# Performance work log

Measured on AMD Instinct MI355X. Metric: run time of the kernel, lower is better.

## Reference

```python
import jax, jax.numpy as jnp
import numpy as np

B, INDIM, OUTDIM = 1024, 2048, 4096


def setup_inputs() -> dict:
    key = jax.random.key(0)
    kx, kw, kb = jax.random.split(key, 3)
    x = jax.random.normal(kx, (B, INDIM), dtype=jnp.float32)
    # nn.Linear(indim, outdim): weight [outdim, indim], bias [outdim]
    bound = 1.0 / np.sqrt(INDIM)
    W = jax.random.uniform(kw, (OUTDIM, INDIM), minval=-bound, maxval=bound, dtype=jnp.float32)
    b = jax.random.uniform(kb, (OUTDIM,), minval=-bound, maxval=bound, dtype=jnp.float32)
    return {"x": x, "W": W, "b": b}


def reference(x, W, b):
    # Faithful to torch: prototypes = weight.transpose(0,1).reshape(outdim, indim)
    # (a reflatten of W^T, not the original weight rows, since outdim != indim).
    protos = W.T.reshape(W.shape[0], W.shape[1])  # [outdim, indim]
    # -||x_i - p_j||^2 - b_j via GEMM identity (same math as broadcast subtract + norm^2)
    x_sq = jnp.sum(x * x, axis=1, keepdims=True)          # [B, 1]
    p_sq = jnp.sum(protos * protos, axis=1)[None, :]      # [1, outdim]
    xp = jnp.einsum('bd,od->bo', x, protos)               # [B, outdim]
    return -(x_sq - 2.0 * xp + p_sq) - b[None, :]
```

## Files before the change

kernel.cpp:

```cpp
#include <hip/hip_runtime.h>

#define IN_DIM  2048
#define OUT_DIM 4096

typedef float     f32x4 __attribute__((ext_vector_type(4)));
typedef long long llx2  __attribute__((ext_vector_type(2)));

__device__ __forceinline__ unsigned int pk4(float a, float b, float c, float d) {
    int v = __builtin_amdgcn_cvt_pk_fp8_f32(a, b, 0, false);
    v     = __builtin_amdgcn_cvt_pk_fp8_f32(c, d, v, true);
    return (unsigned int)v;
}

__device__ __forceinline__ void async16(const void* g, void* l) {
    __builtin_amdgcn_global_load_lds(
        (const __attribute__((address_space(1))) unsigned int*)g,
        (__attribute__((address_space(3))) unsigned int*)l,
        16, 0, 0);
}

__device__ __forceinline__ int gmem_of(int c) { return 2 * (c & 3) + (c >> 2); }

extern "C" __global__ __launch_bounds__(256) void prep(
        const float* __restrict__ W, const float* __restrict__ x,
        unsigned char* __restrict__ protos, unsigned char* __restrict__ xb,
        float* __restrict__ psq_part, float* __restrict__ x_sq) {
    __shared__ float tile[64][65];
    const int t = threadIdx.x;

    if (blockIdx.z == 2) {
        const int b = blockIdx.x + 32 * blockIdx.y;
        const float* xp = x + (size_t)b * IN_DIM + t * 8;
        const float4 v0 = ((const float4*)xp)[0];
        const float4 v1 = ((const float4*)xp)[1];
        uint2 pk;
        pk.x = pk4(v0.x, v0.y, v0.z, v0.w);
        pk.y = pk4(v1.x, v1.y, v1.z, v1.w);
        *(uint2*)(xb + (size_t)b * IN_DIM + (t >> 3) * 64 + gmem_of(t & 7) * 8) = pk;

        float s = v0.x * v0.x + v0.y * v0.y + v0.z * v0.z + v0.w * v0.w
                + v1.x * v1.x + v1.y * v1.y + v1.z * v1.z + v1.w * v1.w;
#pragma unroll
        for (int off = 32; off > 0; off >>= 1) s += __shfl_down(s, off);
        const int lane = t & 63, w = t >> 6;
        if (lane == 0) tile[0][w] = s;
        __syncthreads();
        if (t == 0) x_sq[b] = tile[0][0] + tile[0][1] + tile[0][2] + tile[0][3];
        return;
    }

    const int r  = blockIdx.z;
    const int c0 = blockIdx.x * 64;
    const int d0 = blockIdx.y * 64;
    const int g  = t >> 4;
    const int cc = (t & 15) * 4;

    const float* Wp = W + (size_t)(r * IN_DIM + d0 + g) * IN_DIM + c0 + cc;
#pragma unroll
    for (int p = 0; p < 4; ++p) {
        const float4 v = *(const float4*)(Wp + (size_t)(16 * p) * IN_DIM);
        const int dl = g + 16 * p;
        tile[dl][cc]     = v.x;
        tile[dl][cc + 1] = v.y;
        tile[dl][cc + 2] = v.z;
        tile[dl][cc + 3] = v.w;
    }
    __syncthreads();

    const int c8 = t & 7;
    const int gm = gmem_of(c8);
#pragma unroll
    for (int p = 0; p < 2; ++p) {
        const int cr = (t >> 3) + 32 * p;
        float v[8];
        float ss = 0.f;
#pragma unroll
        for (int j = 0; j < 8; ++j) {
            v[j] = tile[8 * c8 + j][cr];
            ss += v[j] * v[j];
        }
        const int o = 2 * (c0 + cr) + r;
        uint2 pk;
        pk.x = pk4(16.f * v[0], 16.f * v[1], 16.f * v[2], 16.f * v[3]);
        pk.y = pk4(16.f * v[4], 16.f * v[5], 16.f * v[6], 16.f * v[7]);
        *(uint2*)(protos + (size_t)o * IN_DIM + d0 + gm * 8) = pk;
        ss += __shfl_xor(ss, 1);
        ss += __shfl_xor(ss, 2);
        ss += __shfl_xor(ss, 4);
        if (c8 == 0) psq_part[(size_t)blockIdx.y * OUT_DIM + o] = ss;
    }
}

extern "C" __global__ __launch_bounds__(256, 4) void gemm_epi(
        const unsigned char* __restrict__ A,
        const unsigned char* __restrict__ Bt,
        const float* __restrict__ x_sq,
        const float* __restrict__ psq_part,
        const float* __restrict__ bias,
        float* __restrict__ out) {
    __shared__ __align__(16) unsigned char smem[16384];
    unsigned char* lA = smem;
    unsigned char* lB = smem + 8192;

    const int lid = blockIdx.x;
    const int xcd = lid & 7;
    const int wi  = lid >> 3;
    const int nt  = xcd * 8 + (wi & 7);
    const int mt  = wi >> 3;
    const int m0 = mt * 64;
    const int n0 = nt * 64;

    const int t = threadIdx.x;
    const int rS = t >> 3;
    const int pS = t & 7;
    const int lS = pS ^ (rS & 7);
    const size_t goff = (size_t)(lS >> 2) * 1024 + (lS & 3) * 16;
    const unsigned char* gA0 = A  + (size_t)(m0 + rS) * IN_DIM + goff;
    const unsigned char* gA1 = gA0 + (size_t)32 * IN_DIM;
    const unsigned char* gB0 = Bt + (size_t)(n0 + rS) * IN_DIM + goff;
    const unsigned char* gB1 = gB0 + (size_t)32 * IN_DIM;
    unsigned char* lAd = lA + t * 16;
    unsigned char* lBd = lB + t * 16;

    const int wave = t >> 6;
    const int lane = t & 63;
    const int kh = wave & 1;
    const int nh = wave >> 1;
    const int ln = lane & 15;
    const int qd = lane >> 4;
    const int pr = (kh * 4 + qd) ^ (ln & 7);

    f32x4 acc[4][2] = {};

    for (int it = 0; it < 16; ++it) {
        async16(gA0, lAd); async16(gA1, lAd + 4096);
        async16(gB0, lBd); async16(gB1, lBd + 4096);
        gA0 += 64; gA1 += 64; gB0 += 64; gB1 += 64;
        __syncthreads();

        llx2 af[4], bf[2];
#pragma unroll
        for (int i = 0; i < 4; ++i)
            af[i] = *(const llx2*)(lA + (i * 16 + ln) * 128 + pr * 16);
#pragma unroll
        for (int j = 0; j < 2; ++j)
            bf[j] = *(const llx2*)(lB + (nh * 32 + j * 16 + ln) * 128 + pr * 16);
#pragma unroll
        for (int kk = 0; kk < 2; ++kk)
#pragma unroll
            for (int i = 0; i < 4; ++i)
#pragma unroll
                for (int j = 0; j < 2; ++j)
                    acc[i][j] = __builtin_amdgcn_mfma_f32_16x16x32_fp8_fp8(
                                    af[i][kk], bf[j][kk], acc[i][j], 0, 0, 0);
        __syncthreads();
    }

    if (kh == 1) {
#pragma unroll
        for (int i = 0; i < 4; ++i)
#pragma unroll
            for (int j = 0; j < 2; ++j)
                *(f32x4*)(smem + nh * 8192 + (i * 2 + j) * 1024 + lane * 16) =
                    acc[i][j];
    }
    __syncthreads();
    if (kh == 0) {
#pragma unroll
        for (int j = 0; j < 2; ++j) {
            const int col = n0 + nh * 32 + j * 16 + ln;
            float pb = bias[col];
#pragma unroll
            for (int dt = 0; dt < 32; ++dt)
                pb += psq_part[(size_t)dt * OUT_DIM + col];
#pragma unroll
            for (int i = 0; i < 4; ++i) {
                const f32x4 o4 = *(const f32x4*)(smem + nh * 8192 +
                                                 (i * 2 + j) * 1024 + lane * 16);
                const int row0 = m0 + i * 16 + qd * 4;
#pragma unroll
                for (int rr = 0; rr < 4; ++rr) {
                    const int row = row0 + rr;
                    out[(size_t)row * OUT_DIM + col] =
                        0.125f * (acc[i][j][rr] + o4[rr]) - x_sq[row] - pb;
                }
            }
        }
    }
}

extern "C" void kernel_launch(void* const* d_in, const int* in_sizes, int n_in,
                              void* d_out, int out_size, void* d_ws, size_t ws_size,
                              hipStream_t stream) {
    const float* x    = (const float*)d_in[0];
    const float* W    = (const float*)d_in[1];
    const float* bias = (const float*)d_in[2];
    float* out = (float*)d_out;

    char* ws = (char*)d_ws;
    unsigned char* protos = (unsigned char*)ws;
    unsigned char* xb     = (unsigned char*)(ws + (size_t)8 * 1024 * 1024);
    float* x_sq           = (float*)(ws + (size_t)10 * 1024 * 1024);
    float* psq_part       = (float*)(ws + (size_t)10 * 1024 * 1024 + 65536);

    prep<<<dim3(32, 32, 3), 256, 0, stream>>>(W, x, protos, xb, psq_part, x_sq);
    gemm_epi<<<dim3(1024), 256, 0, stream>>>(xb, protos, x_sq, psq_part, bias, out);
}
```

Measured before the change: 106.7 us.

## Split K four ways across waves with 256-byte K tiles and cooperative psq reduction

Each of the four waves now computes the full 64x64 output tile over its own quarter of every 256-byte K slice. The per-iteration K step doubles, halving the loop trip count and barrier count, and the prep kernel writes fp8 data in a new 256-byte interleaved layout to match. The epilogue becomes a 4-way cross-wave reduction through LDS, done in two passes over column halves. The bias plus prototype-norm partial sums are now reduced cooperatively by all 256 threads into shared memory instead of 32 serial loads per thread. LDS use doubles to 32KB and each wave holds 16 accumulators, which may reduce occupancy and adds epilogue LDS traffic.

```diff
diff --git a/kernel.cpp b/kernel.cpp
--- a/kernel.cpp
+++ b/kernel.cpp
@@ -19,7 +19,11 @@
         16, 0, 0);
 }
 
-__device__ __forceinline__ int gmem_of(int c) { return 2 * (c & 3) + (c >> 2); }
+__device__ __forceinline__ int goff8(int c) {
+    const int cl  = c & 31;
+    const int blk = cl >> 2, qd = cl & 3;
+    return (c >> 5) * 256 + ((blk >> 1) * 4 + qd) * 16 + (blk & 1) * 8;
+}
 
 extern "C" __global__ __launch_bounds__(256) void prep(
         const float* __restrict__ W, const float* __restrict__ x,
@@ -36,7 +40,7 @@
         uint2 pk;
         pk.x = pk4(v0.x, v0.y, v0.z, v0.w);
         pk.y = pk4(v1.x, v1.y, v1.z, v1.w);
-        *(uint2*)(xb + (size_t)b * IN_DIM + (t >> 3) * 64 + gmem_of(t & 7) * 8) = pk;
+        *(uint2*)(xb + (size_t)b * IN_DIM + goff8(t)) = pk;
 
         float s = v0.x * v0.x + v0.y * v0.y + v0.z * v0.z + v0.w * v0.w
                 + v1.x * v1.x + v1.y * v1.y + v1.z * v1.z + v1.w * v1.w;
@@ -68,7 +72,7 @@
     __syncthreads();
 
     const int c8 = t & 7;
-    const int gm = gmem_of(c8);
+    const int go = goff8((d0 >> 3) + c8);
 #pragma unroll
     for (int p = 0; p < 2; ++p) {
         const int cr = (t >> 3) + 32 * p;
@@ -83,7 +87,7 @@
         uint2 pk;
         pk.x = pk4(16.f * v[0], 16.f * v[1], 16.f * v[2], 16.f * v[3]);
         pk.y = pk4(16.f * v[4], 16.f * v[5], 16.f * v[6], 16.f * v[7]);
-        *(uint2*)(protos + (size_t)o * IN_DIM + d0 + gm * 8) = pk;
+        *(uint2*)(protos + (size_t)o * IN_DIM + go) = pk;
         ss += __shfl_xor(ss, 1);
         ss += __shfl_xor(ss, 2);
         ss += __shfl_xor(ss, 4);
@@ -98,9 +102,10 @@
         const float* __restrict__ psq_part,
         const float* __restrict__ bias,
         float* __restrict__ out) {
-    __shared__ __align__(16) unsigned char smem[16384];
+    __shared__ __align__(16) unsigned char smem[32768];
+    __shared__ float psb_s[64];
     unsigned char* lA = smem;
-    unsigned char* lB = smem + 8192;
+    unsigned char* lB = smem + 16384;
 
     const int lid = blockIdx.x;
     const int xcd = lid & 7;
@@ -111,80 +116,88 @@
     const int n0 = nt * 64;
 
     const int t = threadIdx.x;
-    const int rS = t >> 3;
-    const int pS = t & 7;
-    const int lS = pS ^ (rS & 7);
-    const size_t goff = (size_t)(lS >> 2) * 1024 + (lS & 3) * 16;
-    const unsigned char* gA0 = A  + (size_t)(m0 + rS) * IN_DIM + goff;
-    const unsigned char* gA1 = gA0 + (size_t)32 * IN_DIM;
-    const unsigned char* gB0 = Bt + (size_t)(n0 + rS) * IN_DIM + goff;
-    const unsigned char* gB1 = gB0 + (size_t)32 * IN_DIM;
-    unsigned char* lAd = lA + t * 16;
-    unsigned char* lBd = lB + t * 16;
-
     const int wave = t >> 6;
     const int lane = t & 63;
-    const int kh = wave & 1;
-    const int nh = wave >> 1;
     const int ln = lane & 15;
     const int qd = lane >> 4;
-    const int pr = (kh * 4 + qd) ^ (ln & 7);
-
-    f32x4 acc[4][2] = {};
-
-    for (int it = 0; it < 16; ++it) {
-        async16(gA0, lAd); async16(gA1, lAd + 4096);
-        async16(gB0, lBd); async16(gB1, lBd + 4096);
-        gA0 += 64; gA1 += 64; gB0 += 64; gB1 += 64;
-        __syncthreads();
-
-        llx2 af[4], bf[2];
+
+    {
+        const int col = n0 + (t >> 2);
+        const int q = t & 3;
+        float s = (q == 0) ? bias[col] : 0.f;
+#pragma unroll
+        for (int dt = 0; dt < 8; ++dt)
+            s += psq_part[(size_t)(8 * q + dt) * OUT_DIM + col];
+        s += __shfl_xor(s, 1);
+        s += __shfl_xor(s, 2);
+        if (q == 0) psb_s[t >> 2] = s;
+    }
+
+    const int rS = t >> 4;
+    const int lS = (t & 15) ^ rS;
+    const unsigned char* gA = A  + (size_t)(m0 + rS) * IN_DIM + lS * 16;
+    const unsigned char* gB = Bt + (size_t)(n0 + rS) * IN_DIM + lS * 16;
+
+    const int pbase = wave * 4 + qd;
+
+    f32x4 acc[4][4] = {};
+
+    for (int it = 0; it < 8; ++it) {
+#pragma unroll
+        for (int j = 0; j < 4; ++j) {
+            async16(gA + (size_t)(16 * j) * IN_DIM + it * 256, lA + j * 4096 + t * 16);
+            async16(gB + (size_t)(16 * j) * IN_DIM + it * 256, lB + j * 4096 + t * 16);
+        }
+        __syncthreads();
+
+        llx2 af[4], bf[4];
 #pragma unroll
         for (int i = 0; i < 4; ++i)
-            af[i] = *(const llx2*)(lA + (i * 16 + ln) * 128 + pr * 16);
-#pragma unroll
-        for (int j = 0; j < 2; ++j)
-            bf[j] = *(const llx2*)(lB + (nh * 32 + j * 16 + ln) * 128 + pr * 16);
+            af[i] = *(const llx2*)(lA + (i * 16 + ln) * 256 + ((pbase ^ ln) * 16));
+#pragma unroll
+        for (int j = 0; j < 4; ++j)
+            bf[j] = *(const llx2*)(lB + (j * 16 + ln) * 256 + ((pbase ^ ln) * 16));
 #pragma unroll
         for (int kk = 0; kk < 2; ++kk)
 #pragma unroll
             for (int i = 0; i < 4; ++i)
 #pragma unroll
-                for (int j = 0; j < 2; ++j)
+                for (int j = 0; j < 4; ++j)
                     acc[i][j] = __builtin_amdgcn_mfma_f32_16x16x32_fp8_fp8(
                                     af[i][kk], bf[j][kk], acc[i][j], 0, 0, 0);
         __syncthreads();
     }
 
-    if (kh == 1) {
+#pragma unroll
+    for (int jp = 0; jp < 2; ++jp) {
+        if (jp) __syncthreads();
 #pragma unroll
         for (int i = 0; i < 4; ++i)
-#pragma unroll
-            for (int j = 0; j < 2; ++j)
-                *(f32x4*)(smem + nh * 8192 + (i * 2 + j) * 1024 + lane * 16) =
-                    acc[i][j];
-    }
-    __syncthreads();
-    if (kh == 0) {
-#pragma unroll
-        for (int j = 0; j < 2; ++j) {
-            const int col = n0 + nh * 32 + j * 16 + ln;
-            float pb = bias[col];
-#pragma unroll
-            for (int dt = 0; dt < 32; ++dt)
-                pb += psq_part[(size_t)dt * OUT_DIM + col];
-#pragma unroll
-            for (int i = 0; i < 4; ++i) {
-                const f32x4 o4 = *(const f32x4*)(smem + nh * 8192 +
-                                                 (i * 2 + j) * 1024 + lane * 16);
-                const int row0 = m0 + i * 16 + qd * 4;
-#pragma unroll
-                for (int rr = 0; rr < 4; ++rr) {
-                    const int row = row0 + rr;
-                    out[(size_t)row * OUT_DIM + col] =
-                        0.125f * (acc[i][j][rr] + o4[rr]) - x_sq[row] - pb;
+            if (i != wave) {
+#pragma unroll
+                for (int jj = 0; jj < 2; ++jj)
+                    *(f32x4*)(smem + (i * 4 + wave) * 2048 + jj * 1024 + lane * 16) =
+                        acc[i][2 * jp + jj];
+            }
+        __syncthreads();
+#pragma unroll
+        for (int jj = 0; jj < 2; ++jj) {
+            const int j = 2 * jp + jj;
+            f32x4 s = acc[wave][j];
+#pragma unroll
+            for (int ww = 0; ww < 4; ++ww)
+                if (ww != wave) {
+                    const f32x4 o4 = *(const f32x4*)(smem + (wave * 4 + ww) * 2048 +
+                                                     jj * 1024 + lane * 16);
+                    s[0] += o4[0]; s[1] += o4[1]; s[2] += o4[2]; s[3] += o4[3];
                 }
-            }
+            const int col = n0 + j * 16 + ln;
+            const float pb = psb_s[j * 16 + ln];
+            const int row0 = m0 + wave * 16 + qd * 4;
+#pragma unroll
+            for (int rr = 0; rr < 4; ++rr)
+                out[(size_t)(row0 + rr) * OUT_DIM + col] =
+                    0.125f * s[rr] - x_sq[row0 + rr] - pb;
         }
     }
 }
```

Result: slower. 236.1 us (+121.3%).
